# Performance work log

Measured on AMD Instinct MI355X. Metric: run time of the kernel, lower is better.

## Reference

```python
import jax, jax.numpy as jnp
import numpy as np

B, N, QD = 2, 4096, 1024
CD = 1024
H, DH = 8, 64
INNER = H * DH  # 512


def setup_inputs() -> dict:
    key = jax.random.key(0)
    ks = jax.random.split(key, 10)
    s = lambda d: (1.0 / np.sqrt(d)).astype(np.float32)
    return {
        "x": jax.random.normal(ks[0], (B, N, QD), dtype=jnp.float32),
        "context": jax.random.normal(ks[1], (B, N, CD), dtype=jnp.float32),
        "mask": jax.random.randint(ks[2], (B, N + 1), 0, 2) > 0,
        # weights stored as [in, out] (y = x @ W), matching torch Linear math
        "Wq": jax.random.normal(ks[3], (QD, INNER), dtype=jnp.float32) * s(QD),
        "Wk": jax.random.normal(ks[4], (CD, INNER), dtype=jnp.float32) * s(CD),
        "Wv": jax.random.normal(ks[5], (CD, INNER), dtype=jnp.float32) * s(CD),
        "Wk_bg": jax.random.normal(ks[6], (QD, INNER), dtype=jnp.float32) * s(QD),
        "Wv_bg": jax.random.normal(ks[7], (QD, INNER), dtype=jnp.float32) * s(QD),
        "Wout": jax.random.normal(ks[8], (INNER, QD), dtype=jnp.float32) * s(INNER),
        "b_out": jax.random.normal(ks[9], (QD,), dtype=jnp.float32) * 0.01,
    }


def reference(x, context, mask, Wq, Wk, Wv, Wk_bg, Wv_bg, Wout, b_out):
    b, n, _ = x.shape
    scale = DH ** -0.5

    q = x @ Wq                                             # [b, n, inner]
    pooled_x = jax.lax.stop_gradient(jnp.mean(x, axis=1, keepdims=True))  # [b, 1, qd]
    k = jnp.concatenate([context @ Wk, pooled_x @ Wk_bg], axis=1)  # [b, n+1, inner]
    v = jnp.concatenate([context @ Wv, pooled_x @ Wv_bg], axis=1)  # [b, n+1, inner]

    split = lambda t: t.reshape(b, t.shape[1], H, DH).transpose(0, 2, 1, 3)  # b h j d
    qh, kh, vh = split(q), split(k), split(v)

    sim = jnp.einsum('bhid,bhjd->bhij', qh, kh) * scale     # [b, h, n, n+1]
    neg = -jnp.finfo(sim.dtype).max
    sim = jnp.where(mask[:, None, None, :], sim, neg)
    attn = jax.nn.softmax(sim, axis=-1)
    out = jnp.einsum('bhij,bhjd->bhid', attn, vh)           # [b, h, n, d]
    out = out.transpose(0, 2, 1, 3).reshape(b, n, INNER)    # [b, n, inner]
    return out @ Wout + b_out                                # dropout p=0 -> identity
```

## Files before the change

kernel.cpp:

```cpp
#include <hip/hip_runtime.h>
#include <stdint.h>

#define N_TOK 4096
#define QDIM  1024
#define CDIM  1024
#define NH    8
#define DH    64
#define INNER 512
#define BATCH 2
#define N1    4097
#define N1P   4128
#define NJB   129
#define VROWS 80
#define PSTRD 20
#define KTILE_SH 2048
#define VTILE_SH 2560

typedef __attribute__((ext_vector_type(8))) short short8;
typedef __attribute__((ext_vector_type(4))) float f32x4;
typedef __attribute__((ext_vector_type(4))) uint32_t u32x4;

__device__ __forceinline__ short f2bf(float f) {
    union { float f; uint32_t u; } x; x.f = f;
    uint32_t r = x.u + 0x7fffu + ((x.u >> 16) & 1u);
    return (short)(r >> 16);
}

__device__ __forceinline__ void async_copy16(void* lds, const void* g) {
    __builtin_amdgcn_global_load_lds(
        (const __attribute__((address_space(1))) void*)g,
        (__attribute__((address_space(3))) void*)lds, 16, 0, 0);
}

__global__ __launch_bounds__(256) void cast2_bf16_kernel(
        const float* __restrict__ a, const float* __restrict__ b,
        short* __restrict__ da, short* __restrict__ db, int n4) {
    int i = blockIdx.x * 256 + threadIdx.x;
    bool first = i < n4;
    const float* s = first ? a : b;
    short* d = first ? da : db;
    int j = first ? i : i - n4;
    float4 v = ((const float4*)s)[j];
    ((short4*)d)[j] = make_short4(f2bf(v.x), f2bf(v.y), f2bf(v.z), f2bf(v.w));
}

__global__ __launch_bounds__(256) void transpose_cast_kernel(
        const float* __restrict__ W, short* __restrict__ Wt, int K, int N,
        float scale) {
    __shared__ float tile[32][33];
    int n0 = blockIdx.x * 32, k0 = blockIdx.y * 32;
    int tx = threadIdx.x & 31, ty = threadIdx.x >> 5;
    for (int r = ty; r < 32; r += 8)
        tile[r][tx] = W[(size_t)(k0 + r) * N + n0 + tx];
    __syncthreads();
    for (int r = ty; r < 32; r += 8)
        Wt[(size_t)(n0 + r) * K + k0 + tx] = f2bf(tile[tx][r] * scale);
}

__global__ __launch_bounds__(256) void pool_partial_kernel(
        const float* __restrict__ x, float* __restrict__ part) {
    int b = blockIdx.y, c = blockIdx.x;
    int t = threadIdx.x;
    float s0 = 0.f, s1 = 0.f, s2 = 0.f, s3 = 0.f;
    const float* xp = x + ((size_t)b * N_TOK + c * 128) * QDIM;
    for (int n = 0; n < 128; n++) {
        const float* row = xp + (size_t)n * QDIM;
        s0 += row[t];
        s1 += row[256 + t];
        s2 += row[512 + t];
        s3 += row[768 + t];
    }
    float* pp = part + ((size_t)b * 32 + c) * QDIM;
    pp[t] = s0; pp[256 + t] = s1; pp[512 + t] = s2; pp[768 + t] = s3;
}

__global__ __launch_bounds__(256) void bg_kernel(
        const float* __restrict__ part, const float* __restrict__ Wkbg,
        const float* __restrict__ Wvbg, short* __restrict__ kb, short* __restrict__ vb) {
    int b = blockIdx.x, jb = blockIdx.y, t = threadIdx.x;
    __shared__ float pooled[QDIM];
    for (int d = t; d < QDIM; d += 256) {
        float s = 0.f;
        for (int c = 0; c < 32; c++) s += part[((size_t)b * 32 + c) * QDIM + d];
        pooled[d] = s * (1.f / (float)N_TOK);
    }
    __syncthreads();
    int flat = jb * 256 + t;
    int matv = flat >> 9;
    int o = flat & 511;
    const float* W = matv ? Wvbg : Wkbg;
    float s = 0.f;
    for (int k = 0; k < QDIM; k++) s += pooled[k] * W[(size_t)k * INNER + o];
    int h = o >> 6, d = o & 63;
    if (matv) {
        vb[(((size_t)(b * NH + h)) * N1P + N_TOK) * DH + d] = f2bf(s);
    } else {
        kb[((size_t)(b * NH + h)) * NJB * KTILE_SH + 128 * KTILE_SH
           + (d >> 5) * 1024 + (d & 31)] = f2bf(s);
    }
    if (jb == 0) {
        for (int idx = t; idx < NH * 31 * DH; idx += 256) {
            int h2 = idx / (31 * DH);
            int r2 = idx % (31 * DH);
            int rr = 1 + r2 / DH;
            int d2 = r2 % DH;
            kb[((size_t)(b * NH + h2)) * NJB * KTILE_SH + 128 * KTILE_SH
               + (d2 >> 5) * 1024 + rr * 32 + (d2 & 31)] = 0;
        }
    }
}

__global__ __launch_bounds__(256) void transpose_v_kernel(
        const short* __restrict__ vin, short* __restrict__ vout,
        const int* __restrict__ mask) {
    __shared__ short tile[32][65];
    __shared__ int mloc[32];
    int bh = blockIdx.z, b = bh >> 3;
    int j0 = blockIdx.x * 32, jb = blockIdx.x;
    int tx = threadIdx.x & 63, ty = threadIdx.x >> 6;
    const short* src = vin + (size_t)bh * N1P * DH;
    for (int r = ty; r < 32; r += 4)
        tile[r][tx] = src[(size_t)(j0 + r) * DH + tx];
    if (threadIdx.x < 32) {
        int j = j0 + threadIdx.x;
        mloc[threadIdx.x] = (j < N1) ? mask[b * N1 + j] : 0;
    }
    __syncthreads();
    int tp = threadIdx.x & 31, dy = threadIdx.x >> 5;
    int s = (tp >> 1) + ((tp & 1) << 4);
    bool mk = mloc[s] != 0;
    short* dst = vout + ((size_t)bh * NJB + jb) * VTILE_SH;
    for (int d = dy; d < DH; d += 8) {
        int swz = (((tp >> 3) ^ ((d >> 1) & 3)) << 3) | (tp & 7);
        dst[d * 32 + swz] = mk ? tile[s][d] : (short)0;
    }
    if (dy == 0) dst[64 * 32 + tp] = mk ? (short)0x3F80 : (short)0;
    if (dy == 1)
        for (int d = 65; d < 80; d++) dst[d * 32 + tp] = 0;
}

__global__ __launch_bounds__(256) void qkv_gemm_kernel(
        const short* __restrict__ x_bf, const short* __restrict__ c_bf,
        const short* __restrict__ Wqt, const short* __restrict__ Wkvt,
        short* __restrict__ q_bf, short* __restrict__ k_bf, short* __restrict__ v_tmp) {
    __shared__ short As[128 * 32];
    __shared__ short Bs[128 * 32];
    const int t = threadIdx.x;
    const int lane = t & 63, w = t >> 6;
    const int wr = w >> 1, wc = w & 1;
    const int lo = lane & 15, g = lane >> 4;
    const int arow = lane >> 2;
    const int ac8 = (lane & 3) * 8;

    const short *A, *W;
    int m0, n0, which;
    int bid = blockIdx.x;
    if (bid < 256) { A = x_bf; W = Wqt;  m0 = (bid >> 2) * 128; n0 = (bid & 3) * 128; which = 0; }
    else { int i = bid - 256; A = c_bf; W = Wkvt; m0 = (i >> 3) * 128; n0 = (i & 7) * 128;
           which = (n0 < 512) ? 1 : 2; }

    f32x4 acc[4][4] = {};
    for (int k0 = 0; k0 < 1024; k0 += 32) {
        for (int q = 0; q < 2; q++) {
            int seg = w * 2 + q;
            async_copy16(&As[seg * 512], A + (size_t)(m0 + seg * 16 + arow) * 1024 + k0 + ac8);
            async_copy16(&Bs[seg * 512], W + (size_t)(n0 + seg * 16 + arow) * 1024 + k0 + ac8);
        }
        __syncthreads();
        short8 af[4], bfv[4];
        #pragma unroll
        for (int i = 0; i < 4; i++)
            af[i] = *(const short8*)&As[(wr * 64 + i * 16 + lo) * 32 + g * 8];
        #pragma unroll
        for (int j = 0; j < 4; j++)
            bfv[j] = *(const short8*)&Bs[(wc * 64 + j * 16 + lo) * 32 + g * 8];
        #pragma unroll
        for (int i = 0; i < 4; i++)
            #pragma unroll
            for (int j = 0; j < 4; j++)
                acc[i][j] = __builtin_amdgcn_mfma_f32_16x16x32_bf16(af[i], bfv[j], acc[i][j], 0, 0, 0);
        __syncthreads();
    }

    if (which == 0) {
        #pragma unroll
        for (int i = 0; i < 4; i++)
            #pragma unroll
            for (int j = 0; j < 4; j++) {
                int row = m0 + wr * 64 + i * 16 + g * 4;
                int col0 = n0 + wc * 64 + j * 16 + lo;
                int h = col0 >> 6, d = col0 & 63;
                f32x4 v = acc[i][j];
                #pragma unroll
                for (int r = 0; r < 4; r++) {
                    int m = row + r;
                    int b = m >> 12, ii = m & 4095;
                    q_bf[(((size_t)(b * NH + h)) * N_TOK + ii) * DH + d] = f2bf(v[r]);
                }
            }
    } else if (which == 1) {
        #pragma unroll
        for (int i = 0; i < 4; i++)
            #pragma unroll
            for (int j = 0; j < 4; j++) {
                int row = m0 + wr * 64 + i * 16 + g * 4;
                int col0 = n0 + wc * 64 + j * 16 + lo;
                int h = col0 >> 6, d = col0 & 63;
                f32x4 v = acc[i][j];
                #pragma unroll
                for (int r = 0; r < 4; r++) {
                    int m = row + r;
                    int b = m >> 12, ii = m & 4095;
                    int off = (d >> 5) * 1024 + (ii & 31) * 32 + (d & 31);
                    off ^= ((ii >> 1) & 3) << 3;
                    k_bf[((size_t)(b * NH + h)) * NJB * KTILE_SH + (ii >> 5) * KTILE_SH
                         + off] = f2bf(v[r]);
                }
            }
    } else {
        #pragma unroll
        for (int i = 0; i < 4; i++)
            #pragma unroll
            for (int j = 0; j < 4; j++) {
                int row = m0 + wr * 64 + i * 16 + g * 4;
                int col0 = n0 + wc * 64 + j * 16 + lo;
                int col = col0 - 512;
                int h = col >> 6, d = col & 63;
                f32x4 v = acc[i][j];
                #pragma unroll
                for (int r = 0; r < 4; r++) {
                    int m = row + r;
                    int b = m >> 12, ii = m & 4095;
                    v_tmp[(((size_t)(b * NH + h)) * N1P + ii) * DH + d] = f2bf(v[r]);
                }
            }
    }
}

__global__ __launch_bounds__(256) void out_gemm_kernel(
        const short* __restrict__ A, const short* __restrict__ Wt,
        float* __restrict__ outf, const float* __restrict__ bias) {
    __shared__ short As[128 * 32];
    __shared__ short Bs[128 * 32];
    const int t = threadIdx.x;
    const int lane = t & 63, w = t >> 6;
    const int wr = w >> 1, wc = w & 1;
    const int lo = lane & 15, g = lane >> 4;
    const int arow = lane >> 2;
    const int ac8 = (lane & 3) * 8;
    const int m0 = blockIdx.x * 128, n0 = blockIdx.y * 128;

    f32x4 acc[4][4] = {};
    for (int k0 = 0; k0 < INNER; k0 += 32) {
        for (int q = 0; q < 2; q++) {
            int seg = w * 2 + q;
            async_copy16(&As[seg * 512], A + (size_t)(m0 + seg * 16 + arow) * INNER + k0 + ac8);
            async_copy16(&Bs[seg * 512], Wt + (size_t)(n0 + seg * 16 + arow) * INNER + k0 + ac8);
        }
        __syncthreads();
        short8 af[4], bfv[4];
        #pragma unroll
        for (int i = 0; i < 4; i++)
            af[i] = *(const short8*)&As[(wr * 64 + i * 16 + lo) * 32 + g * 8];
        #pragma unroll
        for (int j = 0; j < 4; j++)
            bfv[j] = *(const short8*)&Bs[(wc * 64 + j * 16 + lo) * 32 + g * 8];
        #pragma unroll
        for (int i = 0; i < 4; i++)
            #pragma unroll
            for (int j = 0; j < 4; j++)
                acc[i][j] = __builtin_amdgcn_mfma_f32_16x16x32_bf16(af[i], bfv[j], acc[i][j], 0, 0, 0);
        __syncthreads();
    }
    #pragma unroll
    for (int i = 0; i < 4; i++)
        #pragma unroll
        for (int j = 0; j < 4; j++) {
            int row = m0 + wr * 64 + i * 16 + g * 4;
            int col = n0 + wc * 64 + j * 16 + lo;
            f32x4 v = acc[i][j];
            #pragma unroll
            for (int r = 0; r < 4; r++)
                outf[(size_t)(row + r) * QDIM + col] = v[r] + bias[col];
        }
}

__global__ __launch_bounds__(256, 2) void attn_kernel(
        const short* __restrict__ qb,
        const short* __restrict__ kb,
        const short* __restrict__ vtb,
        short* __restrict__ ob) {
    const int t = threadIdx.x, lane = t & 63, w = t >> 6;
    const int lo = lane & 15, g = lane >> 4;
    const int gs = g ^ ((lo >> 1) & 3);
    const int id = blockIdx.x;
    const int h = id & 7, b = (id >> 3) & 1, qt = id >> 4;
    const int q0 = qt * 128 + w * 32;
    const size_t bh = (size_t)(b * NH + h);

    const short* qp = qb + (bh * N_TOK + q0 + lo) * DH;
    short8 qa[2][2];
    qa[0][0] = *(const short8*)(qp + g * 8);
    qa[0][1] = *(const short8*)(qp + 32 + g * 8);
    qa[1][0] = *(const short8*)(qp + 16 * DH + g * 8);
    qa[1][1] = *(const short8*)(qp + 16 * DH + 32 + g * 8);

    __shared__ short Kl[2][KTILE_SH];
    __shared__ short Vl[2][VTILE_SH];
    __shared__ uint32_t Pl[4][32 * PSTRD];

    const short* ksrc = kb + bh * (size_t)NJB * KTILE_SH + w * 512 + lane * 8;
    const short* vsrc = vtb + bh * (size_t)NJB * VTILE_SH + w * 512 + lane * 8;

    f32x4 o[2][5] = {};
    f32x4 z = {};
    uint32_t* pw = &Pl[w][0];

    async_copy16(&Kl[0][w * 512], ksrc);
    async_copy16(&Vl[0][w * 512], vsrc);
    if (w == 0) async_copy16(&Vl[0][2048], vsrc + 2048);
    __syncthreads();

    for (int jb = 0; jb < NJB; ++jb) {
        const int cur = jb & 1;
        if (jb + 1 < NJB) {
            const short* ks = ksrc + (size_t)(jb + 1) * KTILE_SH;
            const short* vs = vsrc + (size_t)(jb + 1) * VTILE_SH;
            async_copy16(&Kl[cur ^ 1][w * 512], ks);
            async_copy16(&Vl[cur ^ 1][w * 512], vs);
            if (w == 0) async_copy16(&Vl[cur ^ 1][2048], vs + 2048);
        }
        const short* kl = &Kl[cur][0];
        short8 kf00 = *(const short8*)&kl[(lo) * 32 + gs * 8];
        short8 kf01 = *(const short8*)&kl[1024 + (lo) * 32 + gs * 8];
        short8 kf10 = *(const short8*)&kl[(16 + lo) * 32 + gs * 8];
        short8 kf11 = *(const short8*)&kl[1024 + (16 + lo) * 32 + gs * 8];
        #pragma unroll
        for (int rg = 0; rg < 2; rg++) {
            f32x4 s0 = __builtin_amdgcn_mfma_f32_16x16x32_bf16(qa[rg][0], kf00, z, 0, 0, 0);
            s0 = __builtin_amdgcn_mfma_f32_16x16x32_bf16(qa[rg][1], kf01, s0, 0, 0, 0);
            f32x4 s1 = __builtin_amdgcn_mfma_f32_16x16x32_bf16(qa[rg][0], kf10, z, 0, 0, 0);
            s1 = __builtin_amdgcn_mfma_f32_16x16x32_bf16(qa[rg][1], kf11, s1, 0, 0, 0);
            #pragma unroll
            for (int r = 0; r < 4; r++) {
                uint32_t u0 = __float_as_uint(__builtin_amdgcn_exp2f(s0[r])) + 0x8000u;
                uint32_t u1 = __float_as_uint(__builtin_amdgcn_exp2f(s1[r])) + 0x8000u;
                pw[(rg * 16 + g * 4 + r) * PSTRD + lo] = __builtin_amdgcn_perm(u1, u0, 0x07060302u);
            }
        }
        const short* vl = &Vl[cur][0];
        short8 vfr[5];
        #pragma unroll
        for (int f = 0; f < 5; f++)
            vfr[f] = *(const short8*)&vl[(f * 16 + lo) * 32 + gs * 8];
        #pragma unroll
        for (int rg = 0; rg < 2; rg++) {
            u32x4 prv = *(const u32x4*)&pw[(rg * 16 + lo) * PSTRD + g * 4];
            short8 pa = __builtin_bit_cast(short8, prv);
            #pragma unroll
            for (int f = 0; f < 5; f++)
                o[rg][f] = __builtin_amdgcn_mfma_f32_16x16x32_bf16(pa, vfr[f], o[rg][f], 0, 0, 0);
        }
        __syncthreads();
    }

    short* op = ob + ((size_t)(b * N_TOK) + q0) * INNER + h * DH;
    #pragma unroll
    for (int rg = 0; rg < 2; rg++)
        for (int r = 0; r < 4; r++) {
            float l = __shfl(o[rg][4][r], lane & 48);
            float inv = (l > 0.f) ? 1.f / l : 0.f;
            short* o_ = op + (size_t)(rg * 16 + g * 4 + r) * INNER;
            o_[lo]      = f2bf(o[rg][0][r] * inv);
            o_[16 + lo] = f2bf(o[rg][1][r] * inv);
            o_[32 + lo] = f2bf(o[rg][2][r] * inv);
            o_[48 + lo] = f2bf(o[rg][3][r] * inv);
        }
}

extern "C" void kernel_launch(void* const* d_in, const int* in_sizes, int n_in,
                              void* d_out, int out_size, void* d_ws, size_t ws_size,
                              hipStream_t stream) {
    const float* x    = (const float*)d_in[0];
    const float* ctx  = (const float*)d_in[1];
    const int*   mask = (const int*)d_in[2];
    const float* Wq   = (const float*)d_in[3];
    const float* Wk   = (const float*)d_in[4];
    const float* Wv   = (const float*)d_in[5];
    const float* Wkbg = (const float*)d_in[6];
    const float* Wvbg = (const float*)d_in[7];
    const float* Wout = (const float*)d_in[8];
    const float* bout = (const float*)d_in[9];
    float* out = (float*)d_out;

    char* p = (char*)d_ws;
    auto alloc = [&](size_t b) { char* r = p; p += (b + 255) & ~(size_t)255; return r; };
    short* x_bf  = (short*)alloc((size_t)BATCH * N_TOK * QDIM * 2);
    short* c_bf  = (short*)alloc((size_t)BATCH * N_TOK * CDIM * 2);
    short* Wqt   = (short*)alloc((size_t)INNER * QDIM * 2);
    short* Wkvt  = (short*)alloc((size_t)2 * INNER * CDIM * 2);
    short* Wot   = (short*)alloc((size_t)QDIM * INNER * 2);
    short* q_bf  = (short*)alloc((size_t)BATCH * NH * N_TOK * DH * 2);
    short* k_bf  = (short*)alloc((size_t)BATCH * NH * NJB * KTILE_SH * 2);
    short* v_tmp = (short*)alloc((size_t)BATCH * NH * N1P * DH * 2);
    short* vt_bf = (short*)alloc((size_t)BATCH * NH * NJB * VTILE_SH * 2);
    short* o_bf  = (short*)alloc((size_t)BATCH * N_TOK * INNER * 2);
    float* part  = (float*)alloc((size_t)BATCH * 32 * QDIM * 4);

    const float SCALE_Q = 0.125f * 1.4426950408889634f;

    int n4 = BATCH * N_TOK * QDIM / 4;
    cast2_bf16_kernel<<<(2 * n4 + 255) / 256, 256, 0, stream>>>(x, ctx, x_bf, c_bf, n4);

    transpose_cast_kernel<<<dim3(INNER / 32, QDIM / 32), 256, 0, stream>>>(Wq, Wqt, QDIM, INNER, SCALE_Q);
    transpose_cast_kernel<<<dim3(INNER / 32, CDIM / 32), 256, 0, stream>>>(Wk, Wkvt, CDIM, INNER, 1.f);
    transpose_cast_kernel<<<dim3(INNER / 32, CDIM / 32), 256, 0, stream>>>(Wv, Wkvt + (size_t)INNER * CDIM, CDIM, INNER, 1.f);
    transpose_cast_kernel<<<dim3(QDIM / 32, INNER / 32), 256, 0, stream>>>(Wout, Wot, INNER, QDIM, 1.f);

    pool_partial_kernel<<<dim3(32, BATCH), 256, 0, stream>>>(x, part);

    qkv_gemm_kernel<<<768, 256, 0, stream>>>(x_bf, c_bf, Wqt, Wkvt, q_bf, k_bf, v_tmp);

    bg_kernel<<<dim3(BATCH, 4), 256, 0, stream>>>(part, Wkbg, Wvbg, k_bf, v_tmp);
    transpose_v_kernel<<<dim3(NJB, 1, BATCH * NH), 256, 0, stream>>>(v_tmp, vt_bf, mask);

    attn_kernel<<<512, 256, 0, stream>>>(q_bf, k_bf, vt_bf, o_bf);

    out_gemm_kernel<<<dim3(64, 8), 256, 0, stream>>>(o_bf, Wot, out, bout);
}
```

Baseline: 364.1 us.

## Give each attention wave 64 query rows and fuse weight transpose launches

New measurement: 385.4 us. +5.8%, slower.

```diff
diff --git a/kernel.cpp b/kernel.cpp
--- a/kernel.cpp
+++ b/kernel.cpp
@@ -44,11 +44,21 @@
     ((short4*)d)[j] = make_short4(f2bf(v.x), f2bf(v.y), f2bf(v.z), f2bf(v.w));
 }
 
-__global__ __launch_bounds__(256) void transpose_cast_kernel(
-        const float* __restrict__ W, short* __restrict__ Wt, int K, int N,
-        float scale) {
+__global__ __launch_bounds__(256) void transpose_cast4_kernel(
+        const float* __restrict__ Wq, const float* __restrict__ Wk,
+        const float* __restrict__ Wv, const float* __restrict__ Wout,
+        short* __restrict__ Wqt, short* __restrict__ Wkvt, short* __restrict__ Wot,
+        float scale_q) {
     __shared__ float tile[32][33];
-    int n0 = blockIdx.x * 32, k0 = blockIdx.y * 32;
+    int z = blockIdx.y;
+    const float* W; short* Wt; int K, N; float scale = 1.f;
+    if (z == 0)      { W = Wq;   Wt = Wqt;  K = QDIM;  N = INNER; scale = scale_q; }
+    else if (z == 1) { W = Wk;   Wt = Wkvt; K = CDIM;  N = INNER; }
+    else if (z == 2) { W = Wv;   Wt = Wkvt + (size_t)INNER * CDIM; K = CDIM; N = INNER; }
+    else             { W = Wout; Wt = Wot;  K = INNER; N = QDIM; }
+    int ntn = N >> 5;
+    int bid = blockIdx.x;
+    int n0 = (bid & (ntn - 1)) * 32, k0 = (bid / ntn) * 32;
     int tx = threadIdx.x & 31, ty = threadIdx.x >> 5;
     for (int r = ty; r < 32; r += 8)
         tile[r][tx] = W[(size_t)(k0 + r) * N + n0 + tx];
@@ -285,7 +295,7 @@
         }
 }
 
-__global__ __launch_bounds__(256, 2) void attn_kernel(
+__global__ __launch_bounds__(128, 2) void attn_kernel(
         const short* __restrict__ qb,
         const short* __restrict__ kb,
         const short* __restrict__ vtb,
@@ -295,29 +305,32 @@
     const int gs = g ^ ((lo >> 1) & 3);
     const int id = blockIdx.x;
     const int h = id & 7, b = (id >> 3) & 1, qt = id >> 4;
-    const int q0 = qt * 128 + w * 32;
+    const int q0 = qt * 128 + w * 64;
     const size_t bh = (size_t)(b * NH + h);
 
     const short* qp = qb + (bh * N_TOK + q0 + lo) * DH;
-    short8 qa[2][2];
-    qa[0][0] = *(const short8*)(qp + g * 8);
-    qa[0][1] = *(const short8*)(qp + 32 + g * 8);
-    qa[1][0] = *(const short8*)(qp + 16 * DH + g * 8);
-    qa[1][1] = *(const short8*)(qp + 16 * DH + 32 + g * 8);
+    short8 qa[4][2];
+    #pragma unroll
+    for (int rg = 0; rg < 4; rg++) {
+        qa[rg][0] = *(const short8*)(qp + (size_t)rg * 16 * DH + g * 8);
+        qa[rg][1] = *(const short8*)(qp + (size_t)rg * 16 * DH + 32 + g * 8);
+    }
 
     __shared__ short Kl[2][KTILE_SH];
     __shared__ short Vl[2][VTILE_SH];
-    __shared__ uint32_t Pl[4][32 * PSTRD];
-
-    const short* ksrc = kb + bh * (size_t)NJB * KTILE_SH + w * 512 + lane * 8;
-    const short* vsrc = vtb + bh * (size_t)NJB * VTILE_SH + w * 512 + lane * 8;
-
-    f32x4 o[2][5] = {};
+    __shared__ uint32_t Pl[2][64 * PSTRD];
+
+    const short* ksrc = kb + bh * (size_t)NJB * KTILE_SH + w * 1024 + lane * 8;
+    const short* vsrc = vtb + bh * (size_t)NJB * VTILE_SH + w * 1024 + lane * 8;
+
+    f32x4 o[4][5] = {};
     f32x4 z = {};
     uint32_t* pw = &Pl[w][0];
 
-    async_copy16(&Kl[0][w * 512], ksrc);
-    async_copy16(&Vl[0][w * 512], vsrc);
+    async_copy16(&Kl[0][w * 1024], ksrc);
+    async_copy16(&Kl[0][w * 1024 + 512], ksrc + 512);
+    async_copy16(&Vl[0][w * 1024], vsrc);
+    async_copy16(&Vl[0][w * 1024 + 512], vsrc + 512);
     if (w == 0) async_copy16(&Vl[0][2048], vsrc + 2048);
     __syncthreads();
 
@@ -326,8 +339,10 @@
         if (jb + 1 < NJB) {
             const short* ks = ksrc + (size_t)(jb + 1) * KTILE_SH;
             const short* vs = vsrc + (size_t)(jb + 1) * VTILE_SH;
-            async_copy16(&Kl[cur ^ 1][w * 512], ks);
-            async_copy16(&Vl[cur ^ 1][w * 512], vs);
+            async_copy16(&Kl[cur ^ 1][w * 1024], ks);
+            async_copy16(&Kl[cur ^ 1][w * 1024 + 512], ks + 512);
+            async_copy16(&Vl[cur ^ 1][w * 1024], vs);
+            async_copy16(&Vl[cur ^ 1][w * 1024 + 512], vs + 512);
             if (w == 0) async_copy16(&Vl[cur ^ 1][2048], vs + 2048);
         }
         const short* kl = &Kl[cur][0];
@@ -336,7 +351,7 @@
         short8 kf10 = *(const short8*)&kl[(16 + lo) * 32 + gs * 8];
         short8 kf11 = *(const short8*)&kl[1024 + (16 + lo) * 32 + gs * 8];
         #pragma unroll
-        for (int rg = 0; rg < 2; rg++) {
+        for (int rg = 0; rg < 4; rg++) {
             f32x4 s0 = __builtin_amdgcn_mfma_f32_16x16x32_bf16(qa[rg][0], kf00, z, 0, 0, 0);
             s0 = __builtin_amdgcn_mfma_f32_16x16x32_bf16(qa[rg][1], kf01, s0, 0, 0, 0);
             f32x4 s1 = __builtin_amdgcn_mfma_f32_16x16x32_bf16(qa[rg][0], kf10, z, 0, 0, 0);
@@ -354,7 +369,7 @@
         for (int f = 0; f < 5; f++)
             vfr[f] = *(const short8*)&vl[(f * 16 + lo) * 32 + gs * 8];
         #pragma unroll
-        for (int rg = 0; rg < 2; rg++) {
+        for (int rg = 0; rg < 4; rg++) {
             u32x4 prv = *(const u32x4*)&pw[(rg * 16 + lo) * PSTRD + g * 4];
             short8 pa = __builtin_bit_cast(short8, prv);
             #pragma unroll
@@ -366,7 +381,8 @@
 
     short* op = ob + ((size_t)(b * N_TOK) + q0) * INNER + h * DH;
     #pragma unroll
-    for (int rg = 0; rg < 2; rg++)
+    for (int rg = 0; rg < 4; rg++)
+        #pragma unroll
         for (int r = 0; r < 4; r++) {
             float l = __shfl(o[rg][4][r], lane & 48);
             float inv = (l > 0.f) ? 1.f / l : 0.f;
@@ -412,10 +428,8 @@
     int n4 = BATCH * N_TOK * QDIM / 4;
     cast2_bf16_kernel<<<(2 * n4 + 255) / 256, 256, 0, stream>>>(x, ctx, x_bf, c_bf, n4);
 
-    transpose_cast_kernel<<<dim3(INNER / 32, QDIM / 32), 256, 0, stream>>>(Wq, Wqt, QDIM, INNER, SCALE_Q);
-    transpose_cast_kernel<<<dim3(INNER / 32, CDIM / 32), 256, 0, stream>>>(Wk, Wkvt, CDIM, INNER, 1.f);
-    transpose_cast_kernel<<<dim3(INNER / 32, CDIM / 32), 256, 0, stream>>>(Wv, Wkvt + (size_t)INNER * CDIM, CDIM, INNER, 1.f);
-    transpose_cast_kernel<<<dim3(QDIM / 32, INNER / 32), 256, 0, stream>>>(Wout, Wot, INNER, QDIM, 1.f);
+    transpose_cast4_kernel<<<dim3(512, 4), 256, 0, stream>>>(
+        Wq, Wk, Wv, Wout, Wqt, Wkvt, Wot, SCALE_Q);
 
     pool_partial_kernel<<<dim3(32, BATCH), 256, 0, stream>>>(x, part);
 
@@ -424,7 +438,7 @@
     bg_kernel<<<dim3(BATCH, 4), 256, 0, stream>>>(part, Wkbg, Wvbg, k_bf, v_tmp);
     transpose_v_kernel<<<dim3(NJB, 1, BATCH * NH), 256, 0, stream>>>(v_tmp, vt_bf, mask);
 
-    attn_kernel<<<512, 256, 0, stream>>>(q_bf, k_bf, vt_bf, o_bf);
+    attn_kernel<<<512, 128, 0, stream>>>(q_bf, k_bf, vt_bf, o_bf);
 
     out_gemm_kernel<<<dim3(64, 8), 256, 0, stream>>>(o_bf, Wot, out, bout);
 }
```

## Keep softmax probabilities in registers via transposed QK MFMA, merge weight transposes

Applied to the files above, without the earlier changes.

Result: faster. 337.4 us (-7.3%).

```diff
diff --git a/kernel.cpp b/kernel.cpp
--- a/kernel.cpp
+++ b/kernel.cpp
@@ -12,7 +12,6 @@
 #define N1P   4128
 #define NJB   129
 #define VROWS 80
-#define PSTRD 20
 #define KTILE_SH 2048
 #define VTILE_SH 2560
 
@@ -44,11 +43,21 @@
     ((short4*)d)[j] = make_short4(f2bf(v.x), f2bf(v.y), f2bf(v.z), f2bf(v.w));
 }
 
-__global__ __launch_bounds__(256) void transpose_cast_kernel(
-        const float* __restrict__ W, short* __restrict__ Wt, int K, int N,
-        float scale) {
+__global__ __launch_bounds__(256) void transpose_cast4_kernel(
+        const float* __restrict__ Wq, const float* __restrict__ Wk,
+        const float* __restrict__ Wv, const float* __restrict__ Wout,
+        short* __restrict__ Wqt, short* __restrict__ Wkvt, short* __restrict__ Wot,
+        float scale_q) {
     __shared__ float tile[32][33];
-    int n0 = blockIdx.x * 32, k0 = blockIdx.y * 32;
+    int z = blockIdx.y;
+    const float* W; short* Wt; int K, N; float scale = 1.f;
+    if (z == 0)      { W = Wq;   Wt = Wqt;  K = QDIM;  N = INNER; scale = scale_q; }
+    else if (z == 1) { W = Wk;   Wt = Wkvt; K = CDIM;  N = INNER; }
+    else if (z == 2) { W = Wv;   Wt = Wkvt + (size_t)INNER * CDIM; K = CDIM; N = INNER; }
+    else             { W = Wout; Wt = Wot;  K = INNER; N = QDIM; }
+    int ntn = N >> 5;
+    int bid = blockIdx.x;
+    int n0 = (bid & (ntn - 1)) * 32, k0 = (bid / ntn) * 32;
     int tx = threadIdx.x & 31, ty = threadIdx.x >> 5;
     for (int r = ty; r < 32; r += 8)
         tile[r][tx] = W[(size_t)(k0 + r) * N + n0 + tx];
@@ -127,7 +136,7 @@
     }
     __syncthreads();
     int tp = threadIdx.x & 31, dy = threadIdx.x >> 5;
-    int s = (tp >> 1) + ((tp & 1) << 4);
+    int s = (tp >> 3) * 4 + (tp & 3) + ((tp >> 2) & 1) * 16;
     bool mk = mloc[s] != 0;
     short* dst = vout + ((size_t)bh * NJB + jb) * VTILE_SH;
     for (int d = dy; d < DH; d += 8) {
@@ -307,14 +316,12 @@
 
     __shared__ short Kl[2][KTILE_SH];
     __shared__ short Vl[2][VTILE_SH];
-    __shared__ uint32_t Pl[4][32 * PSTRD];
 
     const short* ksrc = kb + bh * (size_t)NJB * KTILE_SH + w * 512 + lane * 8;
     const short* vsrc = vtb + bh * (size_t)NJB * VTILE_SH + w * 512 + lane * 8;
 
     f32x4 o[2][5] = {};
     f32x4 z = {};
-    uint32_t* pw = &Pl[w][0];
 
     async_copy16(&Kl[0][w * 512], ksrc);
     async_copy16(&Vl[0][w * 512], vsrc);
@@ -335,19 +342,6 @@
         short8 kf01 = *(const short8*)&kl[1024 + (lo) * 32 + gs * 8];
         short8 kf10 = *(const short8*)&kl[(16 + lo) * 32 + gs * 8];
         short8 kf11 = *(const short8*)&kl[1024 + (16 + lo) * 32 + gs * 8];
-        #pragma unroll
-        for (int rg = 0; rg < 2; rg++) {
-            f32x4 s0 = __builtin_amdgcn_mfma_f32_16x16x32_bf16(qa[rg][0], kf00, z, 0, 0, 0);
-            s0 = __builtin_amdgcn_mfma_f32_16x16x32_bf16(qa[rg][1], kf01, s0, 0, 0, 0);
-            f32x4 s1 = __builtin_amdgcn_mfma_f32_16x16x32_bf16(qa[rg][0], kf10, z, 0, 0, 0);
-            s1 = __builtin_amdgcn_mfma_f32_16x16x32_bf16(qa[rg][1], kf11, s1, 0, 0, 0);
-            #pragma unroll
-            for (int r = 0; r < 4; r++) {
-                uint32_t u0 = __float_as_uint(__builtin_amdgcn_exp2f(s0[r])) + 0x8000u;
-                uint32_t u1 = __float_as_uint(__builtin_amdgcn_exp2f(s1[r])) + 0x8000u;
-                pw[(rg * 16 + g * 4 + r) * PSTRD + lo] = __builtin_amdgcn_perm(u1, u0, 0x07060302u);
-            }
-        }
         const short* vl = &Vl[cur][0];
         short8 vfr[5];
         #pragma unroll
@@ -355,8 +349,24 @@
             vfr[f] = *(const short8*)&vl[(f * 16 + lo) * 32 + gs * 8];
         #pragma unroll
         for (int rg = 0; rg < 2; rg++) {
-            u32x4 prv = *(const u32x4*)&pw[(rg * 16 + lo) * PSTRD + g * 4];
-            short8 pa = __builtin_bit_cast(short8, prv);
+            f32x4 s0 = __builtin_amdgcn_mfma_f32_16x16x32_bf16(kf00, qa[rg][0], z, 0, 0, 0);
+            s0 = __builtin_amdgcn_mfma_f32_16x16x32_bf16(kf01, qa[rg][1], s0, 0, 0, 0);
+            f32x4 s1 = __builtin_amdgcn_mfma_f32_16x16x32_bf16(kf10, qa[rg][0], z, 0, 0, 0);
+            s1 = __builtin_amdgcn_mfma_f32_16x16x32_bf16(kf11, qa[rg][1], s1, 0, 0, 0);
+            uint32_t u0 = __float_as_uint(__builtin_amdgcn_exp2f(s0[0])) + 0x8000u;
+            uint32_t u1 = __float_as_uint(__builtin_amdgcn_exp2f(s0[1])) + 0x8000u;
+            uint32_t u2 = __float_as_uint(__builtin_amdgcn_exp2f(s0[2])) + 0x8000u;
+            uint32_t u3 = __float_as_uint(__builtin_amdgcn_exp2f(s0[3])) + 0x8000u;
+            uint32_t u4 = __float_as_uint(__builtin_amdgcn_exp2f(s1[0])) + 0x8000u;
+            uint32_t u5 = __float_as_uint(__builtin_amdgcn_exp2f(s1[1])) + 0x8000u;
+            uint32_t u6 = __float_as_uint(__builtin_amdgcn_exp2f(s1[2])) + 0x8000u;
+            uint32_t u7 = __float_as_uint(__builtin_amdgcn_exp2f(s1[3])) + 0x8000u;
+            u32x4 pr;
+            pr[0] = __builtin_amdgcn_perm(u1, u0, 0x07060302u);
+            pr[1] = __builtin_amdgcn_perm(u3, u2, 0x07060302u);
+            pr[2] = __builtin_amdgcn_perm(u5, u4, 0x07060302u);
+            pr[3] = __builtin_amdgcn_perm(u7, u6, 0x07060302u);
+            short8 pa = __builtin_bit_cast(short8, pr);
             #pragma unroll
             for (int f = 0; f < 5; f++)
                 o[rg][f] = __builtin_amdgcn_mfma_f32_16x16x32_bf16(pa, vfr[f], o[rg][f], 0, 0, 0);
@@ -367,6 +377,7 @@
     short* op = ob + ((size_t)(b * N_TOK) + q0) * INNER + h * DH;
     #pragma unroll
     for (int rg = 0; rg < 2; rg++)
+        #pragma unroll
         for (int r = 0; r < 4; r++) {
             float l = __shfl(o[rg][4][r], lane & 48);
             float inv = (l > 0.f) ? 1.f / l : 0.f;
@@ -412,10 +423,8 @@
     int n4 = BATCH * N_TOK * QDIM / 4;
     cast2_bf16_kernel<<<(2 * n4 + 255) / 256, 256, 0, stream>>>(x, ctx, x_bf, c_bf, n4);
 
-    transpose_cast_kernel<<<dim3(INNER / 32, QDIM / 32), 256, 0, stream>>>(Wq, Wqt, QDIM, INNER, SCALE_Q);
-    transpose_cast_kernel<<<dim3(INNER / 32, CDIM / 32), 256, 0, stream>>>(Wk, Wkvt, CDIM, INNER, 1.f);
-    transpose_cast_kernel<<<dim3(INNER / 32, CDIM / 32), 256, 0, stream>>>(Wv, Wkvt + (size_t)INNER * CDIM, CDIM, INNER, 1.f);
-    transpose_cast_kernel<<<dim3(QDIM / 32, INNER / 32), 256, 0, stream>>>(Wout, Wot, INNER, QDIM, 1.f);
+    transpose_cast4_kernel<<<dim3(512, 4), 256, 0, stream>>>(
+        Wq, Wk, Wv, Wout, Wqt, Wkvt, Wot, SCALE_Q);
 
     pool_partial_kernel<<<dim3(32, BATCH), 256, 0, stream>>>(x, part);
 
```
